# Kernel tuning notes

Measured on AMD Instinct MI355X. Metric: run time of the kernel, lower is better.

The kernel has to match this reference:

```python
import jax, jax.numpy as jnp
import numpy as np

C = 256
C8 = C // 8
B, H, W = 4, 64, 64


def setup_inputs() -> dict:
    key = jax.random.key(0)
    ks = jax.random.split(key, 8)
    s = 0.05
    return {
        "x": jax.random.normal(ks[0], (B, C, H, W), jnp.float32),
        "wq": jax.random.normal(ks[1], (C8, C), jnp.float32) * s,
        "bq": jax.random.normal(ks[2], (C8,), jnp.float32) * s,
        "wk": jax.random.normal(ks[3], (C8, C), jnp.float32) * s,
        "bk": jax.random.normal(ks[4], (C8,), jnp.float32) * s,
        "wv": jax.random.normal(ks[5], (C, C), jnp.float32) * s,
        "bv": jax.random.normal(ks[6], (C,), jnp.float32) * s,
        "gamma": jax.random.normal(ks[7], (1,), jnp.float32),
    }


def reference(x, wq, bq, wk, bk, wv, bv, gamma):
    b, c, h, w = x.shape
    n = h * w
    xf = x.reshape(b, c, n)                                   # [B,C,N]
    # 1x1 convs == channel matmuls
    q = jnp.einsum('dc,bcn->bnd', wq, xf) + bq                # [B,N,C8] (query, permuted)
    k = jnp.einsum('dc,bcn->bdn', wk, xf) + bk[None, :, None]  # [B,C8,N]
    v = jnp.einsum('ec,bcn->ben', wv, xf) + bv[None, :, None]  # [B,C,N]
    # attention[b,i,j] = <q_i, k_j>, softmax over j (no scaling, as in source)
    attn = jax.nn.softmax(jnp.einsum('bnd,bdm->bnm', q, k), axis=-1)  # [B,N,N]
    # out = value @ attn^T : out[b,e,i] = sum_j v[b,e,j] * attn[b,i,j]
    out = jnp.einsum('bej,bij->bei', v, attn).reshape(b, c, h, w)
    return gamma * out + x
```

## Files before the change

kernel.cpp:

```cpp
#include <hip/hip_runtime.h>
#include <math.h>

typedef __attribute__((ext_vector_type(8))) short bf16x8;
typedef __attribute__((ext_vector_type(4))) float f32x4;
typedef unsigned short ushort;
typedef unsigned int uint;

#define CF4(p) (*reinterpret_cast<const float4*>(p))

__device__ __forceinline__ ushort f2bf(float f) {
    uint u = __float_as_uint(f);
    return (ushort)((u + 0x7FFFu + ((u >> 16) & 1u)) >> 16);
}
__device__ __forceinline__ float bf2f(ushort h) {
    return __uint_as_float(((uint)h) << 16);
}

__global__ __launch_bounds__(256) void proj_kernel(
    const float* __restrict__ x,
    const float* __restrict__ wq, const float* __restrict__ bq,
    const float* __restrict__ wk, const float* __restrict__ bk,
    const float* __restrict__ wv, const float* __restrict__ bv,
    ushort* __restrict__ ws)
{
    ushort* qth = ws;
    ushort* qtl = qth + 524288;
    ushort* kth = qtl + 524288;
    ushort* ktl = kth + 524288;
    ushort* vhp = ktl + 524288;
    ushort* vlp = vhp + 4194304;

    __shared__ float Xt[64][260];
    const int t   = threadIdx.x;
    const int blk = blockIdx.x;
    const int b   = blk >> 6;
    const int n0  = (blk & 63) * 64;

    {
        const int tn4 = (t & 15) * 4;
        const int c0  = t >> 4;
        #pragma unroll
        for (int cc = 0; cc < 16; ++cc) {
            const int c = c0 + (cc << 4);
            const float4 xv = CF4(&x[(((size_t)b * 256 + c) << 12) + n0 + tn4]);
            Xt[tn4 + 0][c] = xv.x;
            Xt[tn4 + 1][c] = xv.y;
            Xt[tn4 + 2][c] = xv.z;
            Xt[tn4 + 3][c] = xv.w;
        }
    }
    __syncthreads();

    const int td = t >> 4;
    const int tn = t & 15;

    for (int g = 0; g < 5; ++g) {
        const int d0 = g * 64;
        float acc[4][4];
        #pragma unroll
        for (int i = 0; i < 4; ++i)
            #pragma unroll
            for (int j = 0; j < 4; ++j) acc[i][j] = 0.f;

        const float* wrow[4];
        float bias[4];
        #pragma unroll
        for (int dd = 0; dd < 4; ++dd) {
            const int rr = d0 + td + (dd << 4);
            if (rr < 32)      { wrow[dd] = wq + rr * 256;        bias[dd] = bq[rr]; }
            else if (rr < 64) { wrow[dd] = wk + (rr - 32) * 256; bias[dd] = bk[rr - 32]; }
            else              { wrow[dd] = wv + (rr - 64) * 256; bias[dd] = bv[rr - 64]; }
        }

        for (int c = 0; c < 256; c += 4) {
            float4 w4[4];
            #pragma unroll
            for (int dd = 0; dd < 4; ++dd) w4[dd] = CF4(&wrow[dd][c]);
            #pragma unroll
            for (int nn = 0; nn < 4; ++nn) {
                const float4 xv = CF4(&Xt[tn + (nn << 4)][c]);
                #pragma unroll
                for (int dd = 0; dd < 4; ++dd) {
                    acc[dd][nn] += w4[dd].x * xv.x + w4[dd].y * xv.y
                                 + w4[dd].z * xv.z + w4[dd].w * xv.w;
                }
            }
        }
        #pragma unroll
        for (int dd = 0; dd < 4; ++dd) {
            const int rr = d0 + td + (dd << 4);
            #pragma unroll
            for (int nn = 0; nn < 4; ++nn) {
                const int n = n0 + tn + (nn << 4);
                const float val = acc[dd][nn] + bias[dd];
                const ushort h  = f2bf(val);
                const ushort lo = f2bf(val - bf2f(h));
                if (rr < 32) {
                    const size_t o = ((size_t)(b * 4096 + n)) * 32 + rr;
                    qth[o] = h; qtl[o] = lo;
                } else if (rr < 64) {
                    const size_t o = ((size_t)(b * 4096 + n)) * 32 + (rr - 32);
                    kth[o] = h; ktl[o] = lo;
                } else {
                    const size_t o = ((size_t)(b * 256 + (rr - 64))) * 4096 + n;
                    vhp[o] = h; vlp[o] = lo;
                }
            }
        }
    }
}

__global__ __launch_bounds__(256, 1) void attn_kernel(
    const ushort* __restrict__ ws,
    const float* __restrict__ x,
    const float* __restrict__ gamma,
    float* __restrict__ out)
{
    const ushort* qth = ws;
    const ushort* qtl = qth + 524288;
    const ushort* kth = qtl + 524288;
    const ushort* ktl = kth + 524288;
    const ushort* vhp = ktl + 524288;
    const ushort* vlp = vhp + 4194304;

    __shared__ __align__(16) ushort Ph[4096];
    __shared__ __align__(16) ushort Pl[4096];
    __shared__ float fac_sh[64];
    __shared__ float l_sh[64];

    const int t    = threadIdx.x;
    const int w    = t >> 6;
    const int lane = t & 63;
    const int m    = lane & 15;
    const int gr   = lane >> 4;

    const int blk = blockIdx.x;
    const int e8  = blk & 7;
    const int b   = e8 >> 1;
    const int i0  = ((blk >> 3) + ((e8 & 1) << 5)) << 6;

    const size_t qkbase = (size_t)b * 4096 * 32;
    const size_t vbase  = (size_t)b * 256 * 4096;

    const int iq = i0 + w * 16 + m;
    const bf16x8 qbh = *(const bf16x8*)(qth + qkbase + (size_t)iq * 32 + 8 * gr);
    const bf16x8 qbl = *(const bf16x8*)(qtl + qkbase + (size_t)iq * 32 + 8 * gr);

    f32x4 accv[4][4];
    #pragma unroll
    for (int a = 0; a < 4; ++a)
        #pragma unroll
        for (int c = 0; c < 4; ++c) accv[a][c] = f32x4{0.f, 0.f, 0.f, 0.f};

    float m_run = -INFINITY, l_run = 0.f;
    const int irow = w * 16 + m;

    for (int jt = 0; jt < 64; ++jt) {
        const int j0 = jt << 6;

        bf16x8 kh[4], kl[4];
        #pragma unroll
        for (int mf = 0; mf < 4; ++mf) {
            const size_t ko = qkbase + (size_t)(j0 + mf * 16 + m) * 32 + 8 * gr;
            kh[mf] = *(const bf16x8*)(kth + ko);
            kl[mf] = *(const bf16x8*)(ktl + ko);
        }
        f32x4 st[4];
        #pragma unroll
        for (int mf = 0; mf < 4; ++mf) {
            f32x4 a = {0.f, 0.f, 0.f, 0.f};
            a = __builtin_amdgcn_mfma_f32_16x16x32_bf16(kh[mf], qbh, a, 0, 0, 0);
            a = __builtin_amdgcn_mfma_f32_16x16x32_bf16(kh[mf], qbl, a, 0, 0, 0);
            a = __builtin_amdgcn_mfma_f32_16x16x32_bf16(kl[mf], qbh, a, 0, 0, 0);
            st[mf] = a;
        }
        float tm = st[0][0];
        #pragma unroll
        for (int mf = 0; mf < 4; ++mf)
            #pragma unroll
            for (int r = 0; r < 4; ++r) tm = fmaxf(tm, st[mf][r]);
        tm = fmaxf(tm, __shfl_xor(tm, 16));
        tm = fmaxf(tm, __shfl_xor(tm, 32));
        const float m_new = fmaxf(m_run, tm);
        const float fac   = __expf(m_run - m_new);
        float p[4][4];
        float ts = 0.f;
        #pragma unroll
        for (int mf = 0; mf < 4; ++mf)
            #pragma unroll
            for (int r = 0; r < 4; ++r) {
                p[mf][r] = __expf(st[mf][r] - m_new);
                ts += p[mf][r];
            }
        ts += __shfl_xor(ts, 16);
        ts += __shfl_xor(ts, 32);
        l_run = l_run * fac + ts;
        m_run = m_new;

        #pragma unroll
        for (int mf = 0; mf < 4; ++mf) {
            const int j    = mf * 16 + 4 * gr;
            const int addr = irow * 64 + (j ^ ((irow & 7) << 3));
            ushort h0 = f2bf(p[mf][0]), h1 = f2bf(p[mf][1]);
            ushort h2 = f2bf(p[mf][2]), h3 = f2bf(p[mf][3]);
            ushort l0 = f2bf(p[mf][0] - bf2f(h0)), l1 = f2bf(p[mf][1] - bf2f(h1));
            ushort l2 = f2bf(p[mf][2] - bf2f(h2)), l3 = f2bf(p[mf][3] - bf2f(h3));
            *reinterpret_cast<uint2*>(&Ph[addr]) =
                make_uint2((uint)h0 | ((uint)h1 << 16), (uint)h2 | ((uint)h3 << 16));
            *reinterpret_cast<uint2*>(&Pl[addr]) =
                make_uint2((uint)l0 | ((uint)l1 << 16), (uint)l2 | ((uint)l3 << 16));
        }
        if (gr == 0) fac_sh[irow] = fac;
        __syncthreads();

        float fc[4];
        #pragma unroll
        for (int f = 0; f < 4; ++f) fc[f] = fac_sh[f * 16 + m];
        #pragma unroll
        for (int mf = 0; mf < 4; ++mf)
            #pragma unroll
            for (int f = 0; f < 4; ++f)
                #pragma unroll
                for (int r = 0; r < 4; ++r) accv[mf][f][r] *= fc[f];

        #pragma unroll
        for (int ks = 0; ks < 2; ++ks) {
            bf16x8 pbh[4], pbl[4];
            #pragma unroll
            for (int f = 0; f < 4; ++f) {
                const int i_   = f * 16 + m;
                const int j    = ks * 32 + 8 * gr;
                const int addr = i_ * 64 + (j ^ ((i_ & 7) << 3));
                pbh[f] = *reinterpret_cast<const bf16x8*>(&Ph[addr]);
                pbl[f] = *reinterpret_cast<const bf16x8*>(&Pl[addr]);
            }
            #pragma unroll
            for (int mf = 0; mf < 4; ++mf) {
                const size_t vo = vbase + (size_t)(w * 64 + mf * 16 + m) * 4096
                                + j0 + ks * 32 + 8 * gr;
                const bf16x8 vah = *(const bf16x8*)(vhp + vo);
                const bf16x8 val = *(const bf16x8*)(vlp + vo);
                #pragma unroll
                for (int f = 0; f < 4; ++f) {
                    accv[mf][f] = __builtin_amdgcn_mfma_f32_16x16x32_bf16(vah, pbh[f], accv[mf][f], 0, 0, 0);
                    accv[mf][f] = __builtin_amdgcn_mfma_f32_16x16x32_bf16(vah, pbl[f], accv[mf][f], 0, 0, 0);
                    accv[mf][f] = __builtin_amdgcn_mfma_f32_16x16x32_bf16(val, pbh[f], accv[mf][f], 0, 0, 0);
                }
            }
        }
        __syncthreads();
    }

    if (gr == 0) l_sh[irow] = l_run;
    __syncthreads();

    const float gv = gamma[0];
    float sc[4];
    #pragma unroll
    for (int f = 0; f < 4; ++f) sc[f] = gv / l_sh[f * 16 + m];
    #pragma unroll
    for (int mf = 0; mf < 4; ++mf)
        #pragma unroll
        for (int f = 0; f < 4; ++f)
            #pragma unroll
            for (int r = 0; r < 4; ++r) {
                const int e = w * 64 + mf * 16 + 4 * gr + r;
                const int i = i0 + f * 16 + m;
                const size_t idx = ((size_t)b * 256 + e) * 4096 + i;
                out[idx] = accv[mf][f][r] * sc[f] + x[idx];
            }
}

extern "C" void kernel_launch(void* const* d_in, const int* in_sizes, int n_in,
                              void* d_out, int out_size, void* d_ws, size_t ws_size,
                              hipStream_t stream) {
    const float* x     = (const float*)d_in[0];
    const float* wq    = (const float*)d_in[1];
    const float* bq    = (const float*)d_in[2];
    const float* wk    = (const float*)d_in[3];
    const float* bk    = (const float*)d_in[4];
    const float* bv    = (const float*)d_in[6];
    const float* wv    = (const float*)d_in[5];
    const float* gamma = (const float*)d_in[7];
    float* out  = (float*)d_out;
    ushort* ws  = (ushort*)d_ws;

    proj_kernel<<<256, 256, 0, stream>>>(x, wq, bq, wk, bk, wv, bv, ws);
    attn_kernel<<<256, 256, 0, stream>>>(ws, x, gamma, out);
}
```

Measured before the change: 402.9 us.

## Split attention output channels across two blocks and stage projection stores in LDS

The attention kernel now launches 512 blocks, each covering half the value channels (128 instead of 256). This halves each block's accumulator registers and allows two blocks per CU, at the price of recomputing QK^T and softmax twice per query tile. The projection kernel now stages its bf16 hi/lo outputs in shared memory and writes them to global as coalesced 16-byte vectors instead of scattered 2-byte stores.

```diff
diff --git a/kernel.cpp b/kernel.cpp
--- a/kernel.cpp
+++ b/kernel.cpp
@@ -6,6 +6,7 @@
 typedef unsigned short ushort;
 typedef unsigned int uint;
 
+#define F4(p)  (*reinterpret_cast<float4*>(p))
 #define CF4(p) (*reinterpret_cast<const float4*>(p))
 
 __device__ __forceinline__ ushort f2bf(float f) {
@@ -31,6 +32,9 @@
     ushort* vlp = vhp + 4194304;
 
     __shared__ float Xt[64][260];
+    __shared__ __align__(16) ushort Oh[4096];
+    __shared__ __align__(16) ushort Ol[4096];
+
     const int t   = threadIdx.x;
     const int blk = blockIdx.x;
     const int b   = blk >> 6;
@@ -86,31 +90,54 @@
                 }
             }
         }
+
         #pragma unroll
         for (int dd = 0; dd < 4; ++dd) {
             const int rr = d0 + td + (dd << 4);
             #pragma unroll
             for (int nn = 0; nn < 4; ++nn) {
-                const int n = n0 + tn + (nn << 4);
+                const int nl  = tn + (nn << 4);
                 const float val = acc[dd][nn] + bias[dd];
                 const ushort h  = f2bf(val);
                 const ushort lo = f2bf(val - bf2f(h));
-                if (rr < 32) {
-                    const size_t o = ((size_t)(b * 4096 + n)) * 32 + rr;
-                    qth[o] = h; qtl[o] = lo;
-                } else if (rr < 64) {
-                    const size_t o = ((size_t)(b * 4096 + n)) * 32 + (rr - 32);
-                    kth[o] = h; ktl[o] = lo;
+                int o;
+                if (g == 0) o = (rr < 32) ? nl * 32 + rr : 2048 + nl * 32 + (rr - 32);
+                else        o = (rr - d0) * 64 + nl;
+                Oh[o] = h; Ol[o] = lo;
+            }
+        }
+        __syncthreads();
+
+        if (g == 0) {
+            const size_t qb = ((size_t)(b * 4096 + n0)) * 32;
+            #pragma unroll
+            for (int s = 0; s < 2; ++s) {
+                const int o = t * 16 + s * 8;
+                const float4 vh = F4(&Oh[o]);
+                const float4 vl = F4(&Ol[o]);
+                if (o < 2048) {
+                    F4(&qth[qb + o]) = vh;
+                    F4(&qtl[qb + o]) = vl;
                 } else {
-                    const size_t o = ((size_t)(b * 256 + (rr - 64))) * 4096 + n;
-                    vhp[o] = h; vlp[o] = lo;
+                    F4(&kth[qb + o - 2048]) = vh;
+                    F4(&ktl[qb + o - 2048]) = vl;
                 }
             }
-        }
+        } else {
+            const size_t vb = ((size_t)(b * 256 + (g - 1) * 64)) * 4096 + n0;
+            #pragma unroll
+            for (int s = 0; s < 2; ++s) {
+                const int o  = t * 16 + s * 8;
+                const size_t ga = vb + (size_t)(o >> 6) * 4096 + (o & 63);
+                F4(&vhp[ga]) = F4(&Oh[o]);
+                F4(&vlp[ga]) = F4(&Ol[o]);
+            }
+        }
+        __syncthreads();
     }
 }
 
-__global__ __launch_bounds__(256, 1) void attn_kernel(
+__global__ __launch_bounds__(256, 2) void attn_kernel(
     const ushort* __restrict__ ws,
     const float* __restrict__ x,
     const float* __restrict__ gamma,
@@ -136,8 +163,10 @@
 
     const int blk = blockIdx.x;
     const int e8  = blk & 7;
+    const int g_  = blk >> 3;
     const int b   = e8 >> 1;
-    const int i0  = ((blk >> 3) + ((e8 & 1) << 5)) << 6;
+    const int i0  = ((g_ & 31) + ((e8 & 1) << 5)) << 6;
+    const int ebase = ((g_ >> 5) << 7) + w * 32;
 
     const size_t qkbase = (size_t)b * 4096 * 32;
     const size_t vbase  = (size_t)b * 256 * 4096;
@@ -146,9 +175,9 @@
     const bf16x8 qbh = *(const bf16x8*)(qth + qkbase + (size_t)iq * 32 + 8 * gr);
     const bf16x8 qbl = *(const bf16x8*)(qtl + qkbase + (size_t)iq * 32 + 8 * gr);
 
-    f32x4 accv[4][4];
+    f32x4 accv[2][4];
     #pragma unroll
-    for (int a = 0; a < 4; ++a)
+    for (int a = 0; a < 2; ++a)
         #pragma unroll
         for (int c = 0; c < 4; ++c) accv[a][c] = f32x4{0.f, 0.f, 0.f, 0.f};
 
@@ -217,7 +246,7 @@
         #pragma unroll
         for (int f = 0; f < 4; ++f) fc[f] = fac_sh[f * 16 + m];
         #pragma unroll
-        for (int mf = 0; mf < 4; ++mf)
+        for (int mf = 0; mf < 2; ++mf)
             #pragma unroll
             for (int f = 0; f < 4; ++f)
                 #pragma unroll
@@ -235,8 +264,8 @@
                 pbl[f] = *reinterpret_cast<const bf16x8*>(&Pl[addr]);
             }
             #pragma unroll
-            for (int mf = 0; mf < 4; ++mf) {
-                const size_t vo = vbase + (size_t)(w * 64 + mf * 16 + m) * 4096
+            for (int mf = 0; mf < 2; ++mf) {
+                const size_t vo = vbase + (size_t)(ebase + mf * 16 + m) * 4096
                                 + j0 + ks * 32 + 8 * gr;
                 const bf16x8 vah = *(const bf16x8*)(vhp + vo);
                 const bf16x8 val = *(const bf16x8*)(vlp + vo);
@@ -259,12 +288,12 @@
     #pragma unroll
     for (int f = 0; f < 4; ++f) sc[f] = gv / l_sh[f * 16 + m];
     #pragma unroll
-    for (int mf = 0; mf < 4; ++mf)
+    for (int mf = 0; mf < 2; ++mf)
         #pragma unroll
         for (int f = 0; f < 4; ++f)
             #pragma unroll
             for (int r = 0; r < 4; ++r) {
-                const int e = w * 64 + mf * 16 + 4 * gr + r;
+                const int e = ebase + mf * 16 + 4 * gr + r;
                 const int i = i0 + f * 16 + m;
                 const size_t idx = ((size_t)b * 256 + e) * 4096 + i;
                 out[idx] = accv[mf][f][r] * sc[f] + x[idx];
@@ -279,12 +308,12 @@
     const float* bq    = (const float*)d_in[2];
     const float* wk    = (const float*)d_in[3];
     const float* bk    = (const float*)d_in[4];
+    const float* wv    = (const float*)d_in[5];
     const float* bv    = (const float*)d_in[6];
-    const float* wv    = (const float*)d_in[5];
     const float* gamma = (const float*)d_in[7];
     float* out  = (float*)d_out;
     ushort* ws  = (ushort*)d_ws;
 
     proj_kernel<<<256, 256, 0, stream>>>(x, wq, bq, wk, bk, wv, bv, ws);
-    attn_kernel<<<256, 256, 0, stream>>>(ws, x, gamma, out);
-}
+    attn_kernel<<<512, 256, 0, stream>>>(ws, x, gamma, out);
+}
```

New measurement: 360.3 us. 10.6% less time.
